# Kernel tuning notes

Hardware: AMD Instinct MI355X
Metric: run time of the kernel (lower is better)

Reference implementation:

```python
import jax, jax.numpy as jnp
import numpy as np
from jax import lax

I, H = 10, 20  # input_size, hidden_size (from nn.LSTM(10, 20, 1))


def setup_inputs() -> dict:
    key = jax.random.key(0)
    k0, k1, k2, k3, k4 = jax.random.split(key, 5)
    B, T = 4096, 512
    s = 1.0 / np.sqrt(H)  # PyTorch LSTM init: U(-1/sqrt(H), 1/sqrt(H))
    data = jax.random.normal(k0, (B, T, I), dtype=jnp.float32)
    W_ih = jax.random.uniform(k1, (4 * H, I), minval=-s, maxval=s, dtype=jnp.float32)
    W_hh = jax.random.uniform(k2, (4 * H, H), minval=-s, maxval=s, dtype=jnp.float32)
    b_ih = jax.random.uniform(k3, (4 * H,), minval=-s, maxval=s, dtype=jnp.float32)
    b_hh = jax.random.uniform(k4, (4 * H,), minval=-s, maxval=s, dtype=jnp.float32)
    return {"data": data, "W_ih": W_ih, "W_hh": W_hh, "b_ih": b_ih, "b_hh": b_hh}


def reference(data, W_ih, W_hh, b_ih, b_hh):
    B = data.shape[0]
    h0 = jnp.zeros((B, H), dtype=data.dtype)
    c0 = jnp.zeros((B, H), dtype=data.dtype)
    bias = b_ih + b_hh
    # Precompute input projections for all timesteps in one big GEMM: [T, B, 4H]
    x_proj = jnp.einsum('bti,gi->tbg', data, W_ih) + bias

    def step(carry, xp_t):
        h, c = carry
        gates = xp_t + h @ W_hh.T  # [B, 4H], PyTorch gate order i,f,g,o
        i_g, f_g, g_g, o_g = jnp.split(gates, 4, axis=-1)
        i_g = jax.nn.sigmoid(i_g)
        f_g = jax.nn.sigmoid(f_g)
        g_g = jnp.tanh(g_g)
        o_g = jax.nn.sigmoid(o_g)
        c_new = f_g * c + i_g * g_g
        h_new = o_g * jnp.tanh(c_new)
        # carry sum of h to avoid materializing [T,B,H] twice; but we return h
        return (h_new, c_new), h_new

    _, outs = lax.scan(step, (h0, c0), x_proj)  # outs: [T, B, H]
    return outs.sum()
```

## Files before the change

kernel.cpp:

```cpp
#include <hip/hip_runtime.h>
#include <stdint.h>

#define ISZ 10
#define HSZ 20
#define BSZ 4096
#define TSZ 512
#define BPW 3
#define NBLK ((BSZ + BPW - 1) / BPW)

typedef __fp16 half2_t __attribute__((ext_vector_type(2)));

__device__ __forceinline__ float fdot2(half2_t a, half2_t b, float c) {
    return __builtin_amdgcn_fdot2(a, b, c, false);
}

__global__ __launch_bounds__(64, 2) void lstm_fwd(
    const float* __restrict__ data, const float* __restrict__ Wih,
    const float* __restrict__ Whh, const float* __restrict__ bih,
    const float* __restrict__ bhh, float* __restrict__ partials)
{
    const int lane  = threadIdx.x;
    const int g     = lane / HSZ;
    const int j     = lane - g * HSZ;
    const int batch = blockIdx.x * BPW + g;
    const bool active = (g < BPW) && (batch < BSZ);
    const int bl = active ? batch : 0;

    const float sc[4] = {-1.44269504f, -1.44269504f, 2.88539008f, -1.44269504f};
    half2_t wih2[4][ISZ / 2], whh2[4][HSZ / 2];
    float bias[4];
#pragma unroll
    for (int q = 0; q < 4; ++q) {
        const int row = q * HSZ + j;
#pragma unroll
        for (int i = 0; i < ISZ / 2; ++i) {
            wih2[q][i].x = (__fp16)(sc[q] * Wih[row * ISZ + 2 * i]);
            wih2[q][i].y = (__fp16)(sc[q] * Wih[row * ISZ + 2 * i + 1]);
        }
#pragma unroll
        for (int k = 0; k < HSZ / 2; ++k) {
            whh2[q][k].x = (__fp16)(sc[q] * Whh[row * HSZ + 2 * k]);
            whh2[q][k].y = (__fp16)(sc[q] * Whh[row * HSZ + 2 * k + 1]);
        }
        bias[q] = sc[q] * (bih[row] + bhh[row]);
    }

    int gaddr[HSZ / 2];
#pragma unroll
    for (int k = 0; k < HSZ / 2; ++k) gaddr[k] = (g * HSZ + 2 * k) * 4;

    half2_t h2[HSZ / 2];
#pragma unroll
    for (int k = 0; k < HSZ / 2; ++k) h2[k] = (half2_t)(__fp16)0.f;

    float c = 0.0f, sum = 0.0f;
    const float* xbase = data + (size_t)bl * (TSZ * ISZ);

    half2_t xa[ISZ / 2], xb[ISZ / 2];

    auto loadx = [&](half2_t* dst, int t) {
        const float2* p = (const float2*)(xbase + t * ISZ);
        float2 v0 = p[0], v1 = p[1], v2 = p[2], v3 = p[3], v4 = p[4];
        dst[0] = __builtin_amdgcn_cvt_pkrtz(v0.x, v0.y);
        dst[1] = __builtin_amdgcn_cvt_pkrtz(v1.x, v1.y);
        dst[2] = __builtin_amdgcn_cvt_pkrtz(v2.x, v2.y);
        dst[3] = __builtin_amdgcn_cvt_pkrtz(v3.x, v3.y);
        dst[4] = __builtin_amdgcn_cvt_pkrtz(v4.x, v4.y);
    };

    auto step = [&](const half2_t* x) {
        float acc[4];
#pragma unroll
        for (int q = 0; q < 4; ++q) {
            float ax = bias[q], al = 0.0f, ah = 0.0f;
#pragma unroll
            for (int i = 0; i < ISZ / 2; ++i) ax = fdot2(wih2[q][i], x[i], ax);
#pragma unroll
            for (int k = 0; k < 5; ++k) al = fdot2(whh2[q][k], h2[k], al);
#pragma unroll
            for (int k = 5; k < 10; ++k) ah = fdot2(whh2[q][k], h2[k], ah);
            acc[q] = ax + (al + ah);
        }
        float ig = __builtin_amdgcn_rcpf(1.0f + __builtin_amdgcn_exp2f(acc[0]));
        float fg = __builtin_amdgcn_rcpf(1.0f + __builtin_amdgcn_exp2f(acc[1]));
        float gg = 1.0f - 2.0f * __builtin_amdgcn_rcpf(1.0f + __builtin_amdgcn_exp2f(acc[2]));
        float og = __builtin_amdgcn_rcpf(1.0f + __builtin_amdgcn_exp2f(acc[3]));
        c = fg * c + ig * gg;
        float tc = 1.0f - 2.0f * __builtin_amdgcn_rcpf(1.0f + __builtin_amdgcn_exp2f(2.88539008f * c));
        float hn = og * tc;
        sum += hn;

        __fp16 hf = (__fp16)hn;
        uint32_t bits = (uint32_t)__builtin_bit_cast(uint16_t, hf);
        uint32_t nb   = (uint32_t)__shfl_xor((int)bits, 1, 64);
        uint32_t lo   = (lane & 1) ? nb : bits;
        uint32_t hi   = (lane & 1) ? bits : nb;
        int pair      = (int)(lo | (hi << 16));
#pragma unroll
        for (int k = 0; k < HSZ / 2; ++k)
            h2[k] = __builtin_bit_cast(half2_t,
                        __builtin_amdgcn_ds_bpermute(gaddr[k], pair));
    };

    loadx(xa, 0);
    for (int t = 0; t < TSZ; t += 2) {
        loadx(xb, t + 1);
        step(xa);
        const int t2 = (t + 2 < TSZ) ? (t + 2) : (TSZ - 1);
        loadx(xa, t2);
        step(xb);
    }

    if (!active) sum = 0.0f;
#pragma unroll
    for (int off = 32; off > 0; off >>= 1) sum += __shfl_down(sum, off, 64);
    if (lane == 0) partials[blockIdx.x] = sum;
}

__global__ __launch_bounds__(1024) void reduce_partials(
    const float* __restrict__ partials, float* __restrict__ out)
{
    float s = 0.0f;
    for (int i = threadIdx.x; i < NBLK; i += 1024) s += partials[i];
#pragma unroll
    for (int off = 32; off > 0; off >>= 1) s += __shfl_down(s, off, 64);
    __shared__ float wsum[16];
    const int w = threadIdx.x >> 6;
    if ((threadIdx.x & 63) == 0) wsum[w] = s;
    __syncthreads();
    if (threadIdx.x < 16) {
        float v = wsum[threadIdx.x];
#pragma unroll
        for (int off = 8; off > 0; off >>= 1) v += __shfl_down(v, off, 64);
        if (threadIdx.x == 0) out[0] = v;
    }
}

extern "C" void kernel_launch(void* const* d_in, const int* in_sizes, int n_in,
                              void* d_out, int out_size, void* d_ws, size_t ws_size,
                              hipStream_t stream) {
    const float* data = (const float*)d_in[0];
    const float* Wih  = (const float*)d_in[1];
    const float* Whh  = (const float*)d_in[2];
    const float* bih  = (const float*)d_in[3];
    const float* bhh  = (const float*)d_in[4];
    float* out        = (float*)d_out;
    float* partials   = (float*)d_ws;

    lstm_fwd<<<NBLK, 64, 0, stream>>>(data, Wih, Whh, bih, bhh, partials);
    reduce_partials<<<1, 1024, 0, stream>>>(partials, out);
}
```

Baseline: 266.8 us.

## Process two independent batch chains per wavefront to hide recurrence latency

Each 64-lane wavefront now runs six batch elements as two interleaved groups of three (A and B), so the dependent fdot2, transcendental and cross-lane permute chains of the two groups can overlap and hide each other's latency. The grid shrinks by half. The hidden-state exchange also changes: the fp16 pack via shfl_xor is dropped, and each group now does two fp32 ds_bpermute calls per pair followed by cvt_pkrtz. That doubles the permute count per group, and more live registers may reduce occupancy.

After: 352.0 us. +31.9%, slower.

```diff
diff --git a/kernel.cpp b/kernel.cpp
--- a/kernel.cpp
+++ b/kernel.cpp
@@ -5,8 +5,8 @@
 #define HSZ 20
 #define BSZ 4096
 #define TSZ 512
-#define BPW 3
-#define NBLK ((BSZ + BPW - 1) / BPW)
+#define CPW 6
+#define NBLK ((BSZ + CPW - 1) / CPW)
 
 typedef __fp16 half2_t __attribute__((ext_vector_type(2)));
 
@@ -22,9 +22,12 @@
     const int lane  = threadIdx.x;
     const int g     = lane / HSZ;
     const int j     = lane - g * HSZ;
-    const int batch = blockIdx.x * BPW + g;
-    const bool active = (g < BPW) && (batch < BSZ);
-    const int bl = active ? batch : 0;
+    const int batchA = blockIdx.x * CPW + g;
+    const int batchB = blockIdx.x * CPW + 3 + g;
+    const bool activeA = (g < 3) && (batchA < BSZ);
+    const bool activeB = (g < 3) && (batchB < BSZ);
+    const int blA = activeA ? batchA : 0;
+    const int blB = activeB ? batchB : 0;
 
     const float sc[4] = {-1.44269504f, -1.44269504f, 2.88539008f, -1.44269504f};
     half2_t wih2[4][ISZ / 2], whh2[4][HSZ / 2];
@@ -45,21 +48,23 @@
         bias[q] = sc[q] * (bih[row] + bhh[row]);
     }
 
-    int gaddr[HSZ / 2];
+    const int gbase = g * HSZ * 4;
+
+    half2_t h2A[HSZ / 2], h2B[HSZ / 2];
 #pragma unroll
-    for (int k = 0; k < HSZ / 2; ++k) gaddr[k] = (g * HSZ + 2 * k) * 4;
+    for (int k = 0; k < HSZ / 2; ++k) {
+        h2A[k] = (half2_t)(__fp16)0.f;
+        h2B[k] = (half2_t)(__fp16)0.f;
+    }
 
-    half2_t h2[HSZ / 2];
-#pragma unroll
-    for (int k = 0; k < HSZ / 2; ++k) h2[k] = (half2_t)(__fp16)0.f;
+    float cA = 0.0f, cB = 0.0f, sumA = 0.0f, sumB = 0.0f;
+    const float* xbaseA = data + (size_t)blA * (TSZ * ISZ);
+    const float* xbaseB = data + (size_t)blB * (TSZ * ISZ);
 
-    float c = 0.0f, sum = 0.0f;
-    const float* xbase = data + (size_t)bl * (TSZ * ISZ);
+    half2_t xaA[ISZ / 2], xbA[ISZ / 2], xaB[ISZ / 2], xbB[ISZ / 2];
 
-    half2_t xa[ISZ / 2], xb[ISZ / 2];
-
-    auto loadx = [&](half2_t* dst, int t) {
-        const float2* p = (const float2*)(xbase + t * ISZ);
+    auto loadx = [&](half2_t* dst, const float* xb, int t) {
+        const float2* p = (const float2*)(xb + t * ISZ);
         float2 v0 = p[0], v1 = p[1], v2 = p[2], v3 = p[3], v4 = p[4];
         dst[0] = __builtin_amdgcn_cvt_pkrtz(v0.x, v0.y);
         dst[1] = __builtin_amdgcn_cvt_pkrtz(v1.x, v1.y);
@@ -68,50 +73,73 @@
         dst[4] = __builtin_amdgcn_cvt_pkrtz(v4.x, v4.y);
     };
 
-    auto step = [&](const half2_t* x) {
-        float acc[4];
+    auto step2 = [&](const half2_t* xA, const half2_t* xB) {
+        float accA[4], accB[4];
 #pragma unroll
         for (int q = 0; q < 4; ++q) {
-            float ax = bias[q], al = 0.0f, ah = 0.0f;
+            float axA = bias[q], alA = 0.0f, ahA = 0.0f;
+            float axB = bias[q], alB = 0.0f, ahB = 0.0f;
 #pragma unroll
-            for (int i = 0; i < ISZ / 2; ++i) ax = fdot2(wih2[q][i], x[i], ax);
+            for (int i = 0; i < ISZ / 2; ++i) {
+                axA = fdot2(wih2[q][i], xA[i], axA);
+                axB = fdot2(wih2[q][i], xB[i], axB);
+            }
 #pragma unroll
-            for (int k = 0; k < 5; ++k) al = fdot2(whh2[q][k], h2[k], al);
+            for (int k = 0; k < 5; ++k) {
+                alA = fdot2(whh2[q][k], h2A[k], alA);
+                alB = fdot2(whh2[q][k], h2B[k], alB);
+            }
 #pragma unroll
-            for (int k = 5; k < 10; ++k) ah = fdot2(whh2[q][k], h2[k], ah);
-            acc[q] = ax + (al + ah);
+            for (int k = 5; k < 10; ++k) {
+                ahA = fdot2(whh2[q][k], h2A[k], ahA);
+                ahB = fdot2(whh2[q][k], h2B[k], ahB);
+            }
+            accA[q] = axA + (alA + ahA);
+            accB[q] = axB + (alB + ahB);
         }
-        float ig = __builtin_amdgcn_rcpf(1.0f + __builtin_amdgcn_exp2f(acc[0]));
-        float fg = __builtin_amdgcn_rcpf(1.0f + __builtin_amdgcn_exp2f(acc[1]));
-        float gg = 1.0f - 2.0f * __builtin_amdgcn_rcpf(1.0f + __builtin_amdgcn_exp2f(acc[2]));
-        float og = __builtin_amdgcn_rcpf(1.0f + __builtin_amdgcn_exp2f(acc[3]));
-        c = fg * c + ig * gg;
-        float tc = 1.0f - 2.0f * __builtin_amdgcn_rcpf(1.0f + __builtin_amdgcn_exp2f(2.88539008f * c));
-        float hn = og * tc;
-        sum += hn;
+        float igA = __builtin_amdgcn_rcpf(1.0f + __builtin_amdgcn_exp2f(accA[0]));
+        float igB = __builtin_amdgcn_rcpf(1.0f + __builtin_amdgcn_exp2f(accB[0]));
+        float fgA = __builtin_amdgcn_rcpf(1.0f + __builtin_amdgcn_exp2f(accA[1]));
+        float fgB = __builtin_amdgcn_rcpf(1.0f + __builtin_amdgcn_exp2f(accB[1]));
+        float ggA = 1.0f - 2.0f * __builtin_amdgcn_rcpf(1.0f + __builtin_amdgcn_exp2f(accA[2]));
+        float ggB = 1.0f - 2.0f * __builtin_amdgcn_rcpf(1.0f + __builtin_amdgcn_exp2f(accB[2]));
+        float ogA = __builtin_amdgcn_rcpf(1.0f + __builtin_amdgcn_exp2f(accA[3]));
+        float ogB = __builtin_amdgcn_rcpf(1.0f + __builtin_amdgcn_exp2f(accB[3]));
+        cA = fgA * cA + igA * ggA;
+        cB = fgB * cB + igB * ggB;
+        float tcA = 1.0f - 2.0f * __builtin_amdgcn_rcpf(1.0f + __builtin_amdgcn_exp2f(2.88539008f * cA));
+        float tcB = 1.0f - 2.0f * __builtin_amdgcn_rcpf(1.0f + __builtin_amdgcn_exp2f(2.88539008f * cB));
+        float hnA = ogA * tcA;
+        float hnB = ogB * tcB;
+        sumA += hnA;
+        sumB += hnB;
 
-        __fp16 hf = (__fp16)hn;
-        uint32_t bits = (uint32_t)__builtin_bit_cast(uint16_t, hf);
-        uint32_t nb   = (uint32_t)__shfl_xor((int)bits, 1, 64);
-        uint32_t lo   = (lane & 1) ? nb : bits;
-        uint32_t hi   = (lane & 1) ? bits : nb;
-        int pair      = (int)(lo | (hi << 16));
+        int iA = __builtin_bit_cast(int, hnA);
+        int iB = __builtin_bit_cast(int, hnB);
 #pragma unroll
-        for (int k = 0; k < HSZ / 2; ++k)
-            h2[k] = __builtin_bit_cast(half2_t,
-                        __builtin_amdgcn_ds_bpermute(gaddr[k], pair));
+        for (int k = 0; k < HSZ / 2; ++k) {
+            float eA = __builtin_bit_cast(float, __builtin_amdgcn_ds_bpermute(gbase + 8 * k, iA));
+            float oA = __builtin_bit_cast(float, __builtin_amdgcn_ds_bpermute(gbase + 8 * k + 4, iA));
+            float eB = __builtin_bit_cast(float, __builtin_amdgcn_ds_bpermute(gbase + 8 * k, iB));
+            float oB = __builtin_bit_cast(float, __builtin_amdgcn_ds_bpermute(gbase + 8 * k + 4, iB));
+            h2A[k] = __builtin_amdgcn_cvt_pkrtz(eA, oA);
+            h2B[k] = __builtin_amdgcn_cvt_pkrtz(eB, oB);
+        }
     };
 
-    loadx(xa, 0);
+    loadx(xaA, xbaseA, 0);
+    loadx(xaB, xbaseB, 0);
     for (int t = 0; t < TSZ; t += 2) {
-        loadx(xb, t + 1);
-        step(xa);
+        loadx(xbA, xbaseA, t + 1);
+        loadx(xbB, xbaseB, t + 1);
+        step2(xaA, xaB);
         const int t2 = (t + 2 < TSZ) ? (t + 2) : (TSZ - 1);
-        loadx(xa, t2);
-        step(xb);
+        loadx(xaA, xbaseA, t2);
+        loadx(xaB, xbaseB, t2);
+        step2(xbA, xbB);
     }
 
-    if (!active) sum = 0.0f;
+    float sum = (activeA ? sumA : 0.0f) + (activeB ? sumB : 0.0f);
 #pragma unroll
     for (int off = 32; off > 0; off >>= 1) sum += __shfl_down(sum, off, 64);
     if (lane == 0) partials[blockIdx.x] = sum;
```

## Assign two hidden units per lane to pack six sequences per wavefront

Applied to the files above, without the earlier changes.

Each lane now computes two hidden units (u and u+10), so each sequence occupies 10 lanes and a 64-lane wave handles 6 sequences instead of 3. This halves the number of blocks. The recurrent weights are repacked so that each half2 pairs h[k] with h[k+10], which lets the new hidden pair be packed directly and removes the shfl_xor step before the bpermute broadcast. The cost is twice the per-lane work on the serial critical path and roughly double the weight registers, with launch bounds relaxed to one block.

Measured after the change: 251.5 us. -5.7%, faster.

```diff
diff --git a/kernel.cpp b/kernel.cpp
--- a/kernel.cpp
+++ b/kernel.cpp
@@ -5,8 +5,8 @@
 #define HSZ 20
 #define BSZ 4096
 #define TSZ 512
-#define BPW 3
-#define NBLK ((BSZ + BPW - 1) / BPW)
+#define GPW 6
+#define NBLK ((BSZ + GPW - 1) / GPW)
 
 typedef __fp16 half2_t __attribute__((ext_vector_type(2)));
 
@@ -14,46 +14,45 @@
     return __builtin_amdgcn_fdot2(a, b, c, false);
 }
 
-__global__ __launch_bounds__(64, 2) void lstm_fwd(
+__global__ __launch_bounds__(64, 1) void lstm_fwd(
     const float* __restrict__ data, const float* __restrict__ Wih,
     const float* __restrict__ Whh, const float* __restrict__ bih,
     const float* __restrict__ bhh, float* __restrict__ partials)
 {
     const int lane  = threadIdx.x;
-    const int g     = lane / HSZ;
-    const int j     = lane - g * HSZ;
-    const int batch = blockIdx.x * BPW + g;
-    const bool active = (g < BPW) && (batch < BSZ);
+    const int g     = lane / 10;
+    const int l     = lane - g * 10;
+    const int batch = blockIdx.x * GPW + g;
+    const bool active = (g < GPW) && (batch < BSZ);
     const int bl = active ? batch : 0;
+    const int gq = (g < GPW) ? g : 0;
 
     const float sc[4] = {-1.44269504f, -1.44269504f, 2.88539008f, -1.44269504f};
-    half2_t wih2[4][ISZ / 2], whh2[4][HSZ / 2];
-    float bias[4];
+    half2_t wih2[2][4][ISZ / 2], whh2[2][4][ISZ];
+    float bias[2][4];
 #pragma unroll
-    for (int q = 0; q < 4; ++q) {
-        const int row = q * HSZ + j;
+    for (int s = 0; s < 2; ++s) {
+        const int u = l + 10 * s;
 #pragma unroll
-        for (int i = 0; i < ISZ / 2; ++i) {
-            wih2[q][i].x = (__fp16)(sc[q] * Wih[row * ISZ + 2 * i]);
-            wih2[q][i].y = (__fp16)(sc[q] * Wih[row * ISZ + 2 * i + 1]);
+        for (int q = 0; q < 4; ++q) {
+            const int row = q * HSZ + u;
+#pragma unroll
+            for (int i = 0; i < ISZ / 2; ++i)
+                wih2[s][q][i] = __builtin_amdgcn_cvt_pkrtz(
+                    sc[q] * Wih[row * ISZ + 2 * i], sc[q] * Wih[row * ISZ + 2 * i + 1]);
+#pragma unroll
+            for (int k = 0; k < ISZ; ++k)
+                whh2[s][q][k] = __builtin_amdgcn_cvt_pkrtz(
+                    sc[q] * Whh[row * HSZ + k], sc[q] * Whh[row * HSZ + k + 10]);
+            bias[s][q] = sc[q] * (bih[row] + bhh[row]);
         }
-#pragma unroll
-        for (int k = 0; k < HSZ / 2; ++k) {
-            whh2[q][k].x = (__fp16)(sc[q] * Whh[row * HSZ + 2 * k]);
-            whh2[q][k].y = (__fp16)(sc[q] * Whh[row * HSZ + 2 * k + 1]);
-        }
-        bias[q] = sc[q] * (bih[row] + bhh[row]);
     }
 
-    int gaddr[HSZ / 2];
+    half2_t h2[ISZ];
 #pragma unroll
-    for (int k = 0; k < HSZ / 2; ++k) gaddr[k] = (g * HSZ + 2 * k) * 4;
+    for (int k = 0; k < ISZ; ++k) h2[k] = (half2_t)(__fp16)0.f;
 
-    half2_t h2[HSZ / 2];
-#pragma unroll
-    for (int k = 0; k < HSZ / 2; ++k) h2[k] = (half2_t)(__fp16)0.f;
-
-    float c = 0.0f, sum = 0.0f;
+    float c0 = 0.0f, c1 = 0.0f, sum = 0.0f;
     const float* xbase = data + (size_t)bl * (TSZ * ISZ);
 
     half2_t xa[ISZ / 2], xb[ISZ / 2];
@@ -69,37 +68,42 @@
     };
 
     auto step = [&](const half2_t* x) {
-        float acc[4];
+        float acc[2][4];
 #pragma unroll
-        for (int q = 0; q < 4; ++q) {
-            float ax = bias[q], al = 0.0f, ah = 0.0f;
+        for (int s = 0; s < 2; ++s)
 #pragma unroll
-            for (int i = 0; i < ISZ / 2; ++i) ax = fdot2(wih2[q][i], x[i], ax);
+            for (int q = 0; q < 4; ++q) {
+                float ax = bias[s][q], al = 0.0f, ah = 0.0f;
 #pragma unroll
-            for (int k = 0; k < 5; ++k) al = fdot2(whh2[q][k], h2[k], al);
+                for (int i = 0; i < ISZ / 2; ++i) ax = fdot2(wih2[s][q][i], x[i], ax);
 #pragma unroll
-            for (int k = 5; k < 10; ++k) ah = fdot2(whh2[q][k], h2[k], ah);
-            acc[q] = ax + (al + ah);
-        }
-        float ig = __builtin_amdgcn_rcpf(1.0f + __builtin_amdgcn_exp2f(acc[0]));
-        float fg = __builtin_amdgcn_rcpf(1.0f + __builtin_amdgcn_exp2f(acc[1]));
-        float gg = 1.0f - 2.0f * __builtin_amdgcn_rcpf(1.0f + __builtin_amdgcn_exp2f(acc[2]));
-        float og = __builtin_amdgcn_rcpf(1.0f + __builtin_amdgcn_exp2f(acc[3]));
-        c = fg * c + ig * gg;
-        float tc = 1.0f - 2.0f * __builtin_amdgcn_rcpf(1.0f + __builtin_amdgcn_exp2f(2.88539008f * c));
-        float hn = og * tc;
-        sum += hn;
+                for (int k = 0; k < 5; ++k) al = fdot2(whh2[s][q][k], h2[k], al);
+#pragma unroll
+                for (int k = 5; k < 10; ++k) ah = fdot2(whh2[s][q][k], h2[k], ah);
+                acc[s][q] = ax + (al + ah);
+            }
+        float ig0 = __builtin_amdgcn_rcpf(1.0f + __builtin_amdgcn_exp2f(acc[0][0]));
+        float ig1 = __builtin_amdgcn_rcpf(1.0f + __builtin_amdgcn_exp2f(acc[1][0]));
+        float fg0 = __builtin_amdgcn_rcpf(1.0f + __builtin_amdgcn_exp2f(acc[0][1]));
+        float fg1 = __builtin_amdgcn_rcpf(1.0f + __builtin_amdgcn_exp2f(acc[1][1]));
+        float gg0 = 1.0f - 2.0f * __builtin_amdgcn_rcpf(1.0f + __builtin_amdgcn_exp2f(acc[0][2]));
+        float gg1 = 1.0f - 2.0f * __builtin_amdgcn_rcpf(1.0f + __builtin_amdgcn_exp2f(acc[1][2]));
+        float og0 = __builtin_amdgcn_rcpf(1.0f + __builtin_amdgcn_exp2f(acc[0][3]));
+        float og1 = __builtin_amdgcn_rcpf(1.0f + __builtin_amdgcn_exp2f(acc[1][3]));
+        c0 = fg0 * c0 + ig0 * gg0;
+        c1 = fg1 * c1 + ig1 * gg1;
+        float tc0 = 1.0f - 2.0f * __builtin_amdgcn_rcpf(1.0f + __builtin_amdgcn_exp2f(2.88539008f * c0));
+        float tc1 = 1.0f - 2.0f * __builtin_amdgcn_rcpf(1.0f + __builtin_amdgcn_exp2f(2.88539008f * c1));
+        float hn0 = og0 * tc0;
+        float hn1 = og1 * tc1;
+        sum += hn0 + hn1;
 
-        __fp16 hf = (__fp16)hn;
-        uint32_t bits = (uint32_t)__builtin_bit_cast(uint16_t, hf);
-        uint32_t nb   = (uint32_t)__shfl_xor((int)bits, 1, 64);
-        uint32_t lo   = (lane & 1) ? nb : bits;
-        uint32_t hi   = (lane & 1) ? bits : nb;
-        int pair      = (int)(lo | (hi << 16));
+        half2_t pair = __builtin_amdgcn_cvt_pkrtz(hn0, hn1);
+        int pi = __builtin_bit_cast(int, pair);
 #pragma unroll
-        for (int k = 0; k < HSZ / 2; ++k)
+        for (int k = 0; k < ISZ; ++k)
             h2[k] = __builtin_bit_cast(half2_t,
-                        __builtin_amdgcn_ds_bpermute(gaddr[k], pair));
+                        __builtin_amdgcn_ds_bpermute((gq * 10 + k) * 4, pi));
     };
 
     loadx(xa, 0);
```
